# Performance work log

Measured on AMD Instinct MI355X. Metric: run time of the kernel, lower is better.

The kernel has to match this reference:

```python
import jax, jax.numpy as jnp
import numpy as np
from jax import lax

B, T, F0 = 16, 400, 40
H = 512
E = 512
MSQ = H * H  # 262144


def relu20(v):
    return jnp.clip(v, 0.0, 20.0)


def bn3d(x, g, b, eps=1e-5):
    # BatchNorm1d over (B, T) per channel, training-mode batch stats (biased var)
    m = x.mean(axis=(0, 2), keepdims=True)
    v = x.var(axis=(0, 2), keepdims=True)
    return g[None, :, None] * (x - m) / jnp.sqrt(v + eps) + b[None, :, None]


def bn2d(x, g, b, eps=1e-5):
    m = x.mean(axis=0)
    v = x.var(axis=0)
    return g * (x - m) / jnp.sqrt(v + eps) + b


def conv1d(x, w, b, dil):
    # x: [B,C,T], w: [O,I,K] (torch Conv1d layout), VALID padding
    y = lax.conv_general_dilated(x, w, window_strides=(1,), padding='VALID',
                                 rhs_dilation=(dil,),
                                 dimension_numbers=('NCH', 'OIH', 'NCH'))
    return y + b[None, :, None]


def pointwise(x, w, b):
    # nn.Linear applied per timestep; w: [out,in]
    return jnp.einsum('bct,dc->bdt', x, w) + b[None, :, None]


def setup_inputs():
    key = jax.random.key(0)
    ks = jax.random.split(key, 16)
    s = 0.05
    rn = lambda k, shape: jax.random.normal(k, shape, jnp.float32) * s
    inp = {
        'input_x': jax.random.normal(ks[0], (B, 1, T, F0), jnp.float32),
        'conv1_w': rn(ks[1], (H, F0, 5)), 'conv1_b': rn(ks[2], (H,)),
        'bn1_g': jnp.ones((H,), jnp.float32), 'bn1_b': jnp.zeros((H,), jnp.float32),
        'conv2_w': rn(ks[3], (H, H, 3)), 'conv2_b': rn(ks[4], (H,)),
        'bn2_g': jnp.ones((H,), jnp.float32), 'bn2_b': jnp.zeros((H,), jnp.float32),
        'conv3_w': rn(ks[5], (H, H, 3)), 'conv3_b': rn(ks[6], (H,)),
        'bn3_g': jnp.ones((H,), jnp.float32), 'bn3_b': jnp.zeros((H,), jnp.float32),
        'lin4_w': rn(ks[7], (H, H)), 'lin4_b': rn(ks[8], (H,)),
        'bn4_g': jnp.ones((H,), jnp.float32), 'bn4_b': jnp.zeros((H,), jnp.float32),
        'lin5_w': rn(ks[9], (H, H)), 'lin5_b': rn(ks[10], (H,)),
        'bn5_g': jnp.ones((H,), jnp.float32), 'bn5_b': jnp.zeros((H,), jnp.float32),
        'bot_w': jax.random.normal(ks[11], (H, MSQ), jnp.float32) * 0.002,
        'bot_b': rn(ks[12], (H,)),
        'bnb_g': jnp.ones((H,), jnp.float32), 'bnb_b': jnp.zeros((H,), jnp.float32),
        'emb_w': rn(ks[13], (E, H)), 'emb_b': rn(ks[14], (E,)),
    }
    return inp


def reference(input_x, conv1_w, conv1_b, bn1_g, bn1_b,
              conv2_w, conv2_b, bn2_g, bn2_b,
              conv3_w, conv3_b, bn3_g, bn3_b,
              lin4_w, lin4_b, bn4_g, bn4_b,
              lin5_w, lin5_b, bn5_g, bn5_b,
              bot_w, bot_b, bnb_g, bnb_b,
              emb_w, emb_b):
    # (B,1,T,F) -> (B,F,T)
    x = jnp.transpose(input_x[:, 0], (0, 2, 1))
    x = relu20(bn3d(conv1d(x, conv1_w, conv1_b, 1), bn1_g, bn1_b))   # [B,H,T-4]
    x = relu20(bn3d(conv1d(x, conv2_w, conv2_b, 2), bn2_g, bn2_b))   # [B,H,T-8]
    x = relu20(bn3d(conv1d(x, conv3_w, conv3_b, 4), bn3_g, bn3_b))   # [B,H,T-16]
    x = relu20(bn3d(pointwise(x, lin4_w, lin4_b), bn4_g, bn4_b))     # [B,H,T']
    xb = relu20(bn3d(pointwise(x, lin5_w, lin5_b), bn5_g, bn5_b))    # [B,H,T']
    # M[b] = sum_t outer(x[b,:,t], xb[b,:,t])  == batched GEMM
    m = jnp.einsum('bit,bjt->bij', x, xb).reshape(x.shape[0], -1)    # [B, H*H]
    h = relu20(bn2d(m @ bot_w.T + bot_b, bnb_g, bnb_b))              # [B,H]
    emb = h @ emb_w.T + emb_b                                        # [B,E]
    norm = jnp.sqrt(jnp.sum(emb * emb, axis=1) + 1e-10)
    return (emb / norm[:, None]) * 10.0
```

## Files before the change

### kernel.cpp

```cpp
#include <hip/hip_runtime.h>
#include <math.h>

#define BB 16
#define T0 400
#define HH 512
#define T1 396
#define T2 392
#define T3 384
#define KBOT 262144

typedef __attribute__((ext_vector_type(8))) short bf16x8;
typedef __attribute__((ext_vector_type(4))) float f32x4;

__device__ __forceinline__ short f2bf(float f) {
  unsigned u = __builtin_bit_cast(unsigned, f);
  u += 0x7fff + ((u >> 16) & 1);
  return (short)(u >> 16);
}

#define OFF_Y1  0u
#define OFF_Y2  3244032u
#define OFF_Y3  6455296u
#define OFF_Y4  9601024u
#define OFF_Y5  12746752u
#define OFF_M   15892480u
#define OFF_P   20086784u
#define OFF_PP  22183936u
#define OFF_H   22249472u
#define OFF_SC  22257664u
#define OFF_WPK 22262784u
#define OFF_XB0 23393280u
#define OFF_XB1 23598080u
#define OFF_XB2 25220096u
#define OFF_XB3 26825728u
#define OFF_XB4 28398592u
#define OFF_X4F 29971456u
#define OFF_X5F 31544320u

#define WP1 0
#define WP2 163840
#define WP3 950272
#define WP4 1736704
#define WP5 1998848

__global__ __launch_bounds__(256) void pack_weights(
    const float* __restrict__ w1, const float* __restrict__ w2,
    const float* __restrict__ w3, const float* __restrict__ w4,
    const float* __restrict__ w5, short* __restrict__ dst) {
  const int nelem[5] = {163840, 786432, 786432, 262144, 262144};
  const int kbv[5]   = {10, 48, 48, 16, 16};
  const int offv[5]  = {WP1, WP2, WP3, WP4, WP5};
  int widx = blockIdx.y;
  int f = blockIdx.x * 256 + threadIdx.x;
  if (f >= nelem[widx]) return;
  int j = f & 7, lane = (f >> 3) & 63, rest = f >> 9;
  int KB = kbv[widx];
  int kb = rest % KB, mt = rest / KB;
  int m = mt * 16 + (lane & 15);
  int k = kb * 32 + (lane >> 4) * 8 + j;
  float v;
  if (widx == 0) {
    int kt = k >> 6, fi = k & 63;
    v = (fi < 40) ? w1[m * 200 + fi * 5 + kt] : 0.f;
  } else if (widx <= 2) {
    const float* w = (widx == 1) ? w2 : w3;
    int kt = k >> 9, c = k & 511;
    v = w[m * 1536 + c * 3 + kt];
  } else {
    const float* w = (widx == 3) ? w4 : w5;
    v = w[m * 512 + k];
  }
  dst[offv[widx] + f] = f2bf(v);
}

__global__ __launch_bounds__(256) void convert_in(
    const float* __restrict__ in, short* __restrict__ xb0) {
  int row = blockIdx.x * 4 + (threadIdx.x >> 6);
  int c = threadIdx.x & 63;
  float v = (c < 40) ? in[row * 40 + c] : 0.f;
  xb0[row * 64 + c] = f2bf(v);
}

template <int KTAPS, int DIL, int TIN, int TOUT, int CIN>
__global__ __launch_bounds__(256) void gemm_mfma(
    const short* __restrict__ Wpk, const short* __restrict__ Xb, float* __restrict__ Y) {
  constexpr int KBTOT = KTAPS * CIN / 32;
  __shared__ short Bfrag[4096];
  int tid = threadIdx.x;
  int sn = tid >> 2;
  int cb0 = (tid & 3) * 16;
  int cb1 = cb0 + 8;
  int n_glob = blockIdx.x * 64 + sn;
  int b = n_glob / TOUT, t = n_glob - b * TOUT;
  const short* xrow = Xb + (b * TIN + t) * CIN;
  int wave = tid >> 6, lane = tid & 63;
  int wm = wave >> 1, wn = wave & 1;
  int mt0 = blockIdx.y * 4 + wm * 2;
  const short* a_base0 = Wpk + mt0 * KBTOT * 512 + lane * 8;
  const short* a_base1 = a_base0 + KBTOT * 512;
  int wo0 = (((cb0 >> 5) * 4 + (sn >> 4)) * 64 + (sn & 15) + 16 * ((cb0 & 31) >> 3)) * 8;
  int wo1 = (((cb1 >> 5) * 4 + (sn >> 4)) * 64 + (sn & 15) + 16 * ((cb1 & 31) >> 3)) * 8;
  int ro = wn * 1024 + lane * 8;
  f32x4 acc00 = {0,0,0,0}, acc01 = {0,0,0,0}, acc10 = {0,0,0,0}, acc11 = {0,0,0,0};
  for (int kt = 0; kt < KTAPS; ++kt) {
    const short* xk = xrow + DIL * kt * CIN;
    for (int c0 = 0; c0 < CIN; c0 += 64) {
      bf16x8 v0 = *(const bf16x8*)(xk + c0 + cb0);
      bf16x8 v1 = *(const bf16x8*)(xk + c0 + cb1);
      *(bf16x8*)&Bfrag[wo0] = v0;
      *(bf16x8*)&Bfrag[wo1] = v1;
      __syncthreads();
      int kbase = (kt * CIN + c0) >> 5;
      #pragma unroll
      for (int ks = 0; ks < 2; ++ks) {
        bf16x8 a0 = *(const bf16x8*)(a_base0 + (kbase + ks) * 512);
        bf16x8 a1 = *(const bf16x8*)(a_base1 + (kbase + ks) * 512);
        bf16x8 b0 = *(const bf16x8*)&Bfrag[ro + ks * 2048];
        bf16x8 b1 = *(const bf16x8*)&Bfrag[ro + ks * 2048 + 512];
        acc00 = __builtin_amdgcn_mfma_f32_16x16x32_bf16(a0, b0, acc00, 0, 0, 0);
        acc01 = __builtin_amdgcn_mfma_f32_16x16x32_bf16(a0, b1, acc01, 0, 0, 0);
        acc10 = __builtin_amdgcn_mfma_f32_16x16x32_bf16(a1, b0, acc10, 0, 0, 0);
        acc11 = __builtin_amdgcn_mfma_f32_16x16x32_bf16(a1, b1, acc11, 0, 0, 0);
      }
      __syncthreads();
    }
  }
  int quad = lane >> 4, nl = lane & 15;
  int mb = blockIdx.y * 64 + wm * 32 + quad * 4;
  int nb = blockIdx.x * 64 + wn * 32;
  *(f32x4*)(Y + (nb + nl) * 512 + mb)           = acc00;
  *(f32x4*)(Y + (nb + 16 + nl) * 512 + mb)      = acc01;
  *(f32x4*)(Y + (nb + nl) * 512 + mb + 16)      = acc10;
  *(f32x4*)(Y + (nb + 16 + nl) * 512 + mb + 16) = acc11;
}

__global__ __launch_bounds__(256) void bn_partial(
    const float* __restrict__ Y, int nrows, float* __restrict__ Pp) {
  int tid = threadIdx.x;
  float s0 = 0, s20 = 0, s1 = 0, s21 = 0;
  for (int r = blockIdx.x; r < nrows; r += 64) {
    float v0 = Y[r * 512 + tid];
    float v1 = Y[r * 512 + tid + 256];
    s0 += v0; s20 = fmaf(v0, v0, s20);
    s1 += v1; s21 = fmaf(v1, v1, s21);
  }
  float* base = Pp + blockIdx.x * 1024;
  base[tid] = s0; base[tid + 256] = s1;
  base[512 + tid] = s20; base[512 + tid + 256] = s21;
}

__global__ __launch_bounds__(512) void bn_final(
    const float* __restrict__ Pp, const float* __restrict__ g,
    const float* __restrict__ beta, float n, float* __restrict__ sc, float* __restrict__ sh) {
  int c = threadIdx.x;
  float S = 0, S2 = 0;
  for (int blk = 0; blk < 64; ++blk) {
    S += Pp[blk * 1024 + c];
    S2 += Pp[blk * 1024 + 512 + c];
  }
  float mean = S / n, var = S2 / n - mean * mean;
  float scale = g[c] * rsqrtf(var + 1e-5f);
  sc[c] = scale;
  sh[c] = beta[c] - mean * scale;
}

__global__ __launch_bounds__(256) void bn_apply_bf(
    const float* __restrict__ Y, const float* __restrict__ sc,
    const float* __restrict__ sh, short* __restrict__ Xb) {
  int idx = (blockIdx.x * 256 + threadIdx.x) * 8;
  int c = idx & 511;
  float4 a = *(const float4*)(Y + idx);
  float4 d = *(const float4*)(Y + idx + 4);
  float4 s0 = *(const float4*)(sc + c);
  float4 s1 = *(const float4*)(sc + c + 4);
  float4 h0 = *(const float4*)(sh + c);
  float4 h1 = *(const float4*)(sh + c + 4);
  bf16x8 o;
  o[0] = f2bf(fminf(fmaxf(fmaf(a.x, s0.x, h0.x), 0.f), 20.f));
  o[1] = f2bf(fminf(fmaxf(fmaf(a.y, s0.y, h0.y), 0.f), 20.f));
  o[2] = f2bf(fminf(fmaxf(fmaf(a.z, s0.z, h0.z), 0.f), 20.f));
  o[3] = f2bf(fminf(fmaxf(fmaf(a.w, s0.w, h0.w), 0.f), 20.f));
  o[4] = f2bf(fminf(fmaxf(fmaf(d.x, s1.x, h1.x), 0.f), 20.f));
  o[5] = f2bf(fminf(fmaxf(fmaf(d.y, s1.y, h1.y), 0.f), 20.f));
  o[6] = f2bf(fminf(fmaxf(fmaf(d.z, s1.z, h1.z), 0.f), 20.f));
  o[7] = f2bf(fminf(fmaxf(fmaf(d.w, s1.w, h1.w), 0.f), 20.f));
  *(bf16x8*)(Xb + idx) = o;
}

__global__ __launch_bounds__(256) void apply_frag(
    const float* __restrict__ Y, const float* __restrict__ sc,
    const float* __restrict__ sh, short* __restrict__ Xf) {
  __shared__ float ysm[64][65];
  int tk = blockIdx.x, it = blockIdx.y, b = blockIdx.z;
  int tid = threadIdx.x;
  int ii = (tid & 15) * 4;
  #pragma unroll
  for (int p = 0; p < 4; ++p) {
    int tt = p * 16 + (tid >> 4);
    *(float4*)&ysm[tt][ii] =
        *(const float4*)(Y + ((b * 384) + tk * 64 + tt) * 512 + it * 64 + ii);
  }
  __syncthreads();
  int i_loc = tid & 63;
  int i = it * 64 + i_loc;
  float scale = sc[i], shift = sh[i];
  int mt = it * 4 + (i_loc >> 4);
  #pragma unroll
  for (int p = 0; p < 2; ++p) {
    int tq = p * 4 + (tid >> 6);
    bf16x8 pk;
    #pragma unroll
    for (int j = 0; j < 8; ++j) {
      float v = fmaf(ysm[tq * 8 + j][i_loc], scale, shift);
      pk[j] = f2bf(fminf(fmaxf(v, 0.f), 20.f));
    }
    int kb = tk * 2 + (tq >> 2);
    int lanew = (i_loc & 15) + 16 * (tq & 3);
    *(bf16x8*)(Xf + (((b * 32 + mt) * 12 + kb) * 64 + lanew) * 8) = pk;
  }
}

__global__ __launch_bounds__(256) void outer_mfma(
    const short* __restrict__ Af, const short* __restrict__ Bf, float* __restrict__ M) {
  int b = blockIdx.z;
  int tid = threadIdx.x, wave = tid >> 6, lane = tid & 63;
  int wm = wave >> 1, wn = wave & 1;
  int mt0 = blockIdx.y * 4 + wm * 2;
  int nt0 = blockIdx.x * 4 + wn * 2;
  const short* pa0 = Af + (b * 32 + mt0) * 12 * 512 + lane * 8;
  const short* pa1 = pa0 + 12 * 512;
  const short* pb0 = Bf + (b * 32 + nt0) * 12 * 512 + lane * 8;
  const short* pb1 = pb0 + 12 * 512;
  f32x4 acc00 = {0,0,0,0}, acc01 = {0,0,0,0}, acc10 = {0,0,0,0}, acc11 = {0,0,0,0};
  #pragma unroll 4
  for (int kb = 0; kb < 12; ++kb) {
    bf16x8 a0 = *(const bf16x8*)(pa0 + kb * 512);
    bf16x8 a1 = *(const bf16x8*)(pa1 + kb * 512);
    bf16x8 b0 = *(const bf16x8*)(pb0 + kb * 512);
    bf16x8 b1 = *(const bf16x8*)(pb1 + kb * 512);
    acc00 = __builtin_amdgcn_mfma_f32_16x16x32_bf16(a0, b0, acc00, 0, 0, 0);
    acc01 = __builtin_amdgcn_mfma_f32_16x16x32_bf16(a0, b1, acc01, 0, 0, 0);
    acc10 = __builtin_amdgcn_mfma_f32_16x16x32_bf16(a1, b0, acc10, 0, 0, 0);
    acc11 = __builtin_amdgcn_mfma_f32_16x16x32_bf16(a1, b1, acc11, 0, 0, 0);
  }
  int quad = lane >> 4, nl = lane & 15;
  float* Mb = M + b * 262144;
  int i0 = blockIdx.y * 64 + wm * 32 + quad * 4;
  int j0 = blockIdx.x * 64 + wn * 32 + nl;
  #pragma unroll
  for (int r = 0; r < 4; ++r) {
    Mb[(i0 + r) * 512 + j0]           = acc00[r];
    Mb[(i0 + r) * 512 + j0 + 16]      = acc01[r];
    Mb[(i0 + 16 + r) * 512 + j0]      = acc10[r];
    Mb[(i0 + 16 + r) * 512 + j0 + 16] = acc11[r];
  }
}

__global__ __launch_bounds__(256) void bot_partial_kernel(
    const float* __restrict__ m, const float* __restrict__ W, float* __restrict__ P) {
  __shared__ float Ws[32][128];
  __shared__ float Ms[32][16];
  int ic = blockIdx.x;
  int n0 = blockIdx.y * 128;
  int tid = threadIdx.x;
  int kb = ic * 1024;
  int wr = tid >> 1;
  int wc = (tid & 1) * 16;
  int nl = (tid & 63) * 2;
  int bq = (tid >> 6) * 4;
  float acc[4][2] = {};
  for (int k0 = kb; k0 < kb + 1024; k0 += 32) {
    #pragma unroll
    for (int q = 0; q < 4; ++q) {
      float4 wv = *(const float4*)(W + (n0 + wr) * KBOT + k0 + wc + q * 4);
      Ws[wc + q * 4 + 0][wr] = wv.x; Ws[wc + q * 4 + 1][wr] = wv.y;
      Ws[wc + q * 4 + 2][wr] = wv.z; Ws[wc + q * 4 + 3][wr] = wv.w;
    }
    if (tid < 128) {
      int b = tid >> 3, kg = (tid & 7) * 4;
      float4 mv = *(const float4*)(m + b * KBOT + k0 + kg);
      Ms[kg + 0][b] = mv.x; Ms[kg + 1][b] = mv.y; Ms[kg + 2][b] = mv.z; Ms[kg + 3][b] = mv.w;
    }
    __syncthreads();
    #pragma unroll
    for (int kk = 0; kk < 32; ++kk) {
      float2 w2 = *(const float2*)&Ws[kk][nl];
      float4 m4 = *(const float4*)&Ms[kk][bq];
      acc[0][0] = fmaf(m4.x, w2.x, acc[0][0]); acc[0][1] = fmaf(m4.x, w2.y, acc[0][1]);
      acc[1][0] = fmaf(m4.y, w2.x, acc[1][0]); acc[1][1] = fmaf(m4.y, w2.y, acc[1][1]);
      acc[2][0] = fmaf(m4.z, w2.x, acc[2][0]); acc[2][1] = fmaf(m4.z, w2.y, acc[2][1]);
      acc[3][0] = fmaf(m4.w, w2.x, acc[3][0]); acc[3][1] = fmaf(m4.w, w2.y, acc[3][1]);
    }
    __syncthreads();
  }
  #pragma unroll
  for (int i = 0; i < 4; ++i) {
    float* row = P + (ic * 16 + bq + i) * 512 + n0;
    *(float2*)&row[nl] = make_float2(acc[i][0], acc[i][1]);
  }
}

__global__ __launch_bounds__(256) void bot_reduce_kernel(
    const float* __restrict__ P, float* __restrict__ h) {
  int idx = blockIdx.x * 256 + threadIdx.x;
  float s[8] = {};
  for (int ic = 0; ic < 256; ic += 8) {
    #pragma unroll
    for (int q = 0; q < 8; ++q) s[q] += P[(ic + q) * 8192 + idx];
  }
  h[idx] = ((s[0] + s[1]) + (s[2] + s[3])) + ((s[4] + s[5]) + (s[6] + s[7]));
}

__global__ __launch_bounds__(512) void final_kernel(
    const float* __restrict__ h, const float* __restrict__ gb, const float* __restrict__ bb,
    const float* __restrict__ embw, const float* __restrict__ embb, float* __restrict__ out) {
  __shared__ float hn[512];
  __shared__ float red[8];
  int b = blockIdx.x, e = threadIdx.x;
  float s = 0.f, s2 = 0.f;
  #pragma unroll
  for (int q = 0; q < BB; ++q) {
    float v = h[q * 512 + e];
    s += v; s2 = fmaf(v, v, s2);
  }
  float mean = s * (1.f / BB);
  float var = s2 * (1.f / BB) - mean * mean;
  float scale = gb[e] * rsqrtf(var + 1e-5f);
  float val = fmaf(h[b * 512 + e] - mean, scale, bb[e]);
  hn[e] = fminf(fmaxf(val, 0.f), 20.f);
  __syncthreads();
  float acc = 0.f;
  const float* wr = embw + e * 512;
  for (int c = 0; c < 512; c += 4) {
    float4 w4 = *(const float4*)(wr + c);
    float4 h4 = *(const float4*)&hn[c];
    acc = fmaf(w4.x, h4.x, acc); acc = fmaf(w4.y, h4.y, acc);
    acc = fmaf(w4.z, h4.z, acc); acc = fmaf(w4.w, h4.w, acc);
  }
  acc += embb[e];
  float sq = acc * acc;
  #pragma unroll
  for (int off = 32; off > 0; off >>= 1) sq += __shfl_down(sq, off);
  if ((e & 63) == 0) red[e >> 6] = sq;
  __syncthreads();
  float tot = 0.f;
  #pragma unroll
  for (int q = 0; q < 8; ++q) tot += red[q];
  float norm = sqrtf(tot + 1e-10f);
  out[b * 512 + e] = acc * (10.f / norm);
}

extern "C" void kernel_launch(void* const* d_in, const int* in_sizes, int n_in,
                              void* d_out, int out_size, void* d_ws, size_t ws_size,
                              hipStream_t stream) {
  const float* input_x = (const float*)d_in[0];
  const float* w1 = (const float*)d_in[1];
  const float* g1 = (const float*)d_in[3];  const float* b1 = (const float*)d_in[4];
  const float* w2 = (const float*)d_in[5];
  const float* g2 = (const float*)d_in[7];  const float* b2 = (const float*)d_in[8];
  const float* w3 = (const float*)d_in[9];
  const float* g3 = (const float*)d_in[11]; const float* b3 = (const float*)d_in[12];
  const float* w4 = (const float*)d_in[13];
  const float* g4 = (const float*)d_in[15]; const float* b4 = (const float*)d_in[16];
  const float* w5 = (const float*)d_in[17];
  const float* g5 = (const float*)d_in[19]; const float* b5 = (const float*)d_in[20];
  const float* botw = (const float*)d_in[21];
  const float* gb = (const float*)d_in[23]; const float* bb = (const float*)d_in[24];
  const float* embw = (const float*)d_in[25]; const float* embb = (const float*)d_in[26];

  float* ws = (float*)d_ws;
  float* y1 = ws + OFF_Y1;
  float* y2 = ws + OFF_Y2;
  float* y3 = ws + OFF_Y3;
  float* y4 = ws + OFF_Y4;
  float* y5 = ws + OFF_Y5;
  float* M  = ws + OFF_M;
  float* P  = ws + OFF_P;
  float* Pp = ws + OFF_PP;
  float* h  = ws + OFF_H;
  float* SC = ws + OFF_SC;
  short* WPK = (short*)(ws + OFF_WPK);
  short* xb0 = (short*)(ws + OFF_XB0);
  short* xb1 = (short*)(ws + OFF_XB1);
  short* xb2 = (short*)(ws + OFF_XB2);
  short* xb3 = (short*)(ws + OFF_XB3);
  short* xb4 = (short*)(ws + OFF_XB4);
  short* x4f = (short*)(ws + OFF_X4F);
  short* x5f = (short*)(ws + OFF_X5F);
  float* out = (float*)d_out;

  pack_weights<<<dim3(3072, 5), 256, 0, stream>>>(w1, w2, w3, w4, w5, WPK);
  convert_in<<<1600, 256, 0, stream>>>(input_x, xb0);

  gemm_mfma<5, 1, 400, 396, 64><<<dim3(99, 8), 256, 0, stream>>>(WPK + WP1, xb0, y1);
  bn_partial<<<64, 256, 0, stream>>>(y1, 6336, Pp);
  bn_final<<<1, 512, 0, stream>>>(Pp, g1, b1, 6336.f, SC + 0, SC + 512);
  bn_apply_bf<<<1584, 256, 0, stream>>>(y1, SC + 0, SC + 512, xb1);

  gemm_mfma<3, 2, 396, 392, 512><<<dim3(98, 8), 256, 0, stream>>>(WPK + WP2, xb1, y2);
  bn_partial<<<64, 256, 0, stream>>>(y2, 6272, Pp);
  bn_final<<<1, 512, 0, stream>>>(Pp, g2, b2, 6272.f, SC + 1024, SC + 1536);
  bn_apply_bf<<<1568, 256, 0, stream>>>(y2, SC + 1024, SC + 1536, xb2);

  gemm_mfma<3, 4, 392, 384, 512><<<dim3(96, 8), 256, 0, stream>>>(WPK + WP3, xb2, y3);
  bn_partial<<<64, 256, 0, stream>>>(y3, 6144, Pp);
  bn_final<<<1, 512, 0, stream>>>(Pp, g3, b3, 6144.f, SC + 2048, SC + 2560);
  bn_apply_bf<<<1536, 256, 0, stream>>>(y3, SC + 2048, SC + 2560, xb3);

  gemm_mfma<1, 0, 384, 384, 512><<<dim3(96, 8), 256, 0, stream>>>(WPK + WP4, xb3, y4);
  bn_partial<<<64, 256, 0, stream>>>(y4, 6144, Pp);
  bn_final<<<1, 512, 0, stream>>>(Pp, g4, b4, 6144.f, SC + 3072, SC + 3584);
  bn_apply_bf<<<1536, 256, 0, stream>>>(y4, SC + 3072, SC + 3584, xb4);

  gemm_mfma<1, 0, 384, 384, 512><<<dim3(96, 8), 256, 0, stream>>>(WPK + WP5, xb4, y5);
  bn_partial<<<64, 256, 0, stream>>>(y5, 6144, Pp);
  bn_final<<<1, 512, 0, stream>>>(Pp, g5, b5, 6144.f, SC + 4096, SC + 4608);

  apply_frag<<<dim3(6, 8, 16), 256, 0, stream>>>(y4, SC + 3072, SC + 3584, x4f);
  apply_frag<<<dim3(6, 8, 16), 256, 0, stream>>>(y5, SC + 4096, SC + 4608, x5f);

  outer_mfma<<<dim3(8, 8, 16), 256, 0, stream>>>(x4f, x5f, M);
  bot_partial_kernel<<<dim3(256, 4), 256, 0, stream>>>(M, botw, P);
  bot_reduce_kernel<<<32, 256, 0, stream>>>(P, h);
  final_kernel<<<16, 512, 0, stream>>>(h, gb, bb, embw, embb, out);
}
```

Measured before the change: 1.093 ms.

## Fuse BN statistics into GEMM epilogue, double-buffer GEMM, prefetch bottleneck loads

The conv/pointwise GEMMs now reduce per-channel sum and sum-of-squares in their epilogue and write per-block partials. A last-block-done atomic counter lets the final block compute BN scale and shift, which removes the separate bn_partial and bn_final launches and their re-read of Y. The GEMM main loop is double-buffered in LDS with register prefetch of the next A/B fragments, and the two apply_frag launches are merged into one grid. The bottleneck partial kernel also prefetches the next W/M tile into registers before the inner FMA loop. The trade-offs are an extra threadfence and atomic per GEMM block, and a serial tail where one block reduces all partials.

```diff
diff --git a/kernel.cpp b/kernel.cpp
--- a/kernel.cpp
+++ b/kernel.cpp
@@ -74,7 +74,8 @@
 }
 
 __global__ __launch_bounds__(256) void convert_in(
-    const float* __restrict__ in, short* __restrict__ xb0) {
+    const float* __restrict__ in, short* __restrict__ xb0, unsigned* __restrict__ cnt) {
+  if (blockIdx.x == 0 && threadIdx.x == 0) *cnt = 0u;
   int row = blockIdx.x * 4 + (threadIdx.x >> 6);
   int c = threadIdx.x & 63;
   float v = (c < 40) ? in[row * 40 + c] : 0.f;
@@ -83,9 +84,14 @@
 
 template <int KTAPS, int DIL, int TIN, int TOUT, int CIN>
 __global__ __launch_bounds__(256) void gemm_mfma(
-    const short* __restrict__ Wpk, const short* __restrict__ Xb, float* __restrict__ Y) {
+    const short* __restrict__ Wpk, const short* __restrict__ Xb, float* __restrict__ Y,
+    float* __restrict__ Ps, unsigned* __restrict__ cnt,
+    const float* __restrict__ g, const float* __restrict__ beta, float nfull,
+    float* __restrict__ sc, float* __restrict__ sh) {
   constexpr int KBTOT = KTAPS * CIN / 32;
-  __shared__ short Bfrag[4096];
+  constexpr int NIT = KTAPS * CIN / 64;
+  constexpr int CSEG = CIN / 64;
+  __shared__ short Bfrag[2][4096];
   int tid = threadIdx.x;
   int sn = tid >> 2;
   int cb0 = (tid & 3) * 16;
@@ -102,66 +108,125 @@
   int wo1 = (((cb1 >> 5) * 4 + (sn >> 4)) * 64 + (sn & 15) + 16 * ((cb1 & 31) >> 3)) * 8;
   int ro = wn * 1024 + lane * 8;
   f32x4 acc00 = {0,0,0,0}, acc01 = {0,0,0,0}, acc10 = {0,0,0,0}, acc11 = {0,0,0,0};
-  for (int kt = 0; kt < KTAPS; ++kt) {
-    const short* xk = xrow + DIL * kt * CIN;
-    for (int c0 = 0; c0 < CIN; c0 += 64) {
-      bf16x8 v0 = *(const bf16x8*)(xk + c0 + cb0);
-      bf16x8 v1 = *(const bf16x8*)(xk + c0 + cb1);
-      *(bf16x8*)&Bfrag[wo0] = v0;
-      *(bf16x8*)&Bfrag[wo1] = v1;
-      __syncthreads();
-      int kbase = (kt * CIN + c0) >> 5;
-      #pragma unroll
-      for (int ks = 0; ks < 2; ++ks) {
-        bf16x8 a0 = *(const bf16x8*)(a_base0 + (kbase + ks) * 512);
-        bf16x8 a1 = *(const bf16x8*)(a_base1 + (kbase + ks) * 512);
-        bf16x8 b0 = *(const bf16x8*)&Bfrag[ro + ks * 2048];
-        bf16x8 b1 = *(const bf16x8*)&Bfrag[ro + ks * 2048 + 512];
-        acc00 = __builtin_amdgcn_mfma_f32_16x16x32_bf16(a0, b0, acc00, 0, 0, 0);
-        acc01 = __builtin_amdgcn_mfma_f32_16x16x32_bf16(a0, b1, acc01, 0, 0, 0);
-        acc10 = __builtin_amdgcn_mfma_f32_16x16x32_bf16(a1, b0, acc10, 0, 0, 0);
-        acc11 = __builtin_amdgcn_mfma_f32_16x16x32_bf16(a1, b1, acc11, 0, 0, 0);
-      }
-      __syncthreads();
-    }
-  }
+
+  bf16x8 a00 = *(const bf16x8*)(a_base0);
+  bf16x8 a01 = *(const bf16x8*)(a_base0 + 512);
+  bf16x8 a10 = *(const bf16x8*)(a_base1);
+  bf16x8 a11 = *(const bf16x8*)(a_base1 + 512);
+  {
+    bf16x8 v0 = *(const bf16x8*)(xrow + cb0);
+    bf16x8 v1 = *(const bf16x8*)(xrow + cb1);
+    *(bf16x8*)&Bfrag[0][wo0] = v0;
+    *(bf16x8*)&Bfrag[0][wo1] = v1;
+  }
+  __syncthreads();
+  int cur = 0;
+  #pragma unroll
+  for (int it = 0; it < NIT; ++it) {
+    bf16x8 nv0, nv1, na00, na01, na10, na11;
+    const bool more = (it + 1 < NIT);
+    if (more) {
+      int it1 = it + 1;
+      int kt = it1 / CSEG;
+      int c0 = (it1 - kt * CSEG) * 64;
+      const short* p = xrow + DIL * kt * CIN + c0;
+      nv0 = *(const bf16x8*)(p + cb0);
+      nv1 = *(const bf16x8*)(p + cb1);
+      const short* ab0 = a_base0 + it1 * 1024;
+      const short* ab1 = a_base1 + it1 * 1024;
+      na00 = *(const bf16x8*)(ab0);
+      na01 = *(const bf16x8*)(ab0 + 512);
+      na10 = *(const bf16x8*)(ab1);
+      na11 = *(const bf16x8*)(ab1 + 512);
+    }
+    short* bf = &Bfrag[cur][0];
+    bf16x8 bk0n0 = *(const bf16x8*)(bf + ro);
+    bf16x8 bk0n1 = *(const bf16x8*)(bf + ro + 512);
+    bf16x8 bk1n0 = *(const bf16x8*)(bf + ro + 2048);
+    bf16x8 bk1n1 = *(const bf16x8*)(bf + ro + 2560);
+    acc00 = __builtin_amdgcn_mfma_f32_16x16x32_bf16(a00, bk0n0, acc00, 0, 0, 0);
+    acc01 = __builtin_amdgcn_mfma_f32_16x16x32_bf16(a00, bk0n1, acc01, 0, 0, 0);
+    acc10 = __builtin_amdgcn_mfma_f32_16x16x32_bf16(a10, bk0n0, acc10, 0, 0, 0);
+    acc11 = __builtin_amdgcn_mfma_f32_16x16x32_bf16(a10, bk0n1, acc11, 0, 0, 0);
+    acc00 = __builtin_amdgcn_mfma_f32_16x16x32_bf16(a01, bk1n0, acc00, 0, 0, 0);
+    acc01 = __builtin_amdgcn_mfma_f32_16x16x32_bf16(a01, bk1n1, acc01, 0, 0, 0);
+    acc10 = __builtin_amdgcn_mfma_f32_16x16x32_bf16(a11, bk1n0, acc10, 0, 0, 0);
+    acc11 = __builtin_amdgcn_mfma_f32_16x16x32_bf16(a11, bk1n1, acc11, 0, 0, 0);
+    if (more) {
+      *(bf16x8*)&Bfrag[cur ^ 1][wo0] = nv0;
+      *(bf16x8*)&Bfrag[cur ^ 1][wo1] = nv1;
+      a00 = na00; a01 = na01; a10 = na10; a11 = na11;
+    }
+    __syncthreads();
+    cur ^= 1;
+  }
+
   int quad = lane >> 4, nl = lane & 15;
-  int mb = blockIdx.y * 64 + wm * 32 + quad * 4;
-  int nb = blockIdx.x * 64 + wn * 32;
-  *(f32x4*)(Y + (nb + nl) * 512 + mb)           = acc00;
-  *(f32x4*)(Y + (nb + 16 + nl) * 512 + mb)      = acc01;
-  *(f32x4*)(Y + (nb + nl) * 512 + mb + 16)      = acc10;
-  *(f32x4*)(Y + (nb + 16 + nl) * 512 + mb + 16) = acc11;
-}
-
-__global__ __launch_bounds__(256) void bn_partial(
-    const float* __restrict__ Y, int nrows, float* __restrict__ Pp) {
-  int tid = threadIdx.x;
-  float s0 = 0, s20 = 0, s1 = 0, s21 = 0;
-  for (int r = blockIdx.x; r < nrows; r += 64) {
-    float v0 = Y[r * 512 + tid];
-    float v1 = Y[r * 512 + tid + 256];
-    s0 += v0; s20 = fmaf(v0, v0, s20);
-    s1 += v1; s21 = fmaf(v1, v1, s21);
-  }
-  float* base = Pp + blockIdx.x * 1024;
-  base[tid] = s0; base[tid + 256] = s1;
-  base[512 + tid] = s20; base[512 + tid + 256] = s21;
-}
-
-__global__ __launch_bounds__(512) void bn_final(
-    const float* __restrict__ Pp, const float* __restrict__ g,
-    const float* __restrict__ beta, float n, float* __restrict__ sc, float* __restrict__ sh) {
-  int c = threadIdx.x;
-  float S = 0, S2 = 0;
-  for (int blk = 0; blk < 64; ++blk) {
-    S += Pp[blk * 1024 + c];
-    S2 += Pp[blk * 1024 + 512 + c];
-  }
-  float mean = S / n, var = S2 / n - mean * mean;
-  float scale = g[c] * rsqrtf(var + 1e-5f);
-  sc[c] = scale;
-  sh[c] = beta[c] - mean * scale;
+  int chq = wm * 32 + quad * 4;
+  int mbase = blockIdx.y * 64 + chq;
+  int nb0 = blockIdx.x * 64 + wn * 32;
+  *(f32x4*)(Y + (nb0 + nl) * 512 + mbase)           = acc00;
+  *(f32x4*)(Y + (nb0 + 16 + nl) * 512 + mbase)      = acc01;
+  *(f32x4*)(Y + (nb0 + nl) * 512 + mbase + 16)      = acc10;
+  *(f32x4*)(Y + (nb0 + 16 + nl) * 512 + mbase + 16) = acc11;
+
+  float cs0[4], cq0[4], cs1[4], cq1[4];
+  #pragma unroll
+  for (int r = 0; r < 4; ++r) {
+    cs0[r] = acc00[r] + acc01[r];
+    cq0[r] = acc00[r] * acc00[r] + acc01[r] * acc01[r];
+    cs1[r] = acc10[r] + acc11[r];
+    cq1[r] = acc10[r] * acc10[r] + acc11[r] * acc11[r];
+  }
+  #pragma unroll
+  for (int off = 1; off < 16; off <<= 1) {
+    #pragma unroll
+    for (int r = 0; r < 4; ++r) {
+      cs0[r] += __shfl_xor(cs0[r], off);
+      cq0[r] += __shfl_xor(cq0[r], off);
+      cs1[r] += __shfl_xor(cs1[r], off);
+      cq1[r] += __shfl_xor(cq1[r], off);
+    }
+  }
+  if (nl == 0) {
+    float* prow = Ps + (blockIdx.x * 2 + wn) * 1024 + mbase;
+    #pragma unroll
+    for (int r = 0; r < 4; ++r) {
+      prow[r] = cs0[r];
+      prow[16 + r] = cs1[r];
+      prow[512 + r] = cq0[r];
+      prow[528 + r] = cq1[r];
+    }
+  }
+  __threadfence();
+  __syncthreads();
+  __shared__ unsigned s_done;
+  if (tid == 0)
+    s_done = __hip_atomic_fetch_add(cnt, 1u, __ATOMIC_ACQ_REL, __HIP_MEMORY_SCOPE_AGENT);
+  __syncthreads();
+  unsigned nblk = gridDim.x * gridDim.y;
+  if (s_done == nblk - 1) {
+    __threadfence();
+    if (tid == 0) *cnt = 0u;
+    int npr = gridDim.x * 2;
+    int c = tid * 2;
+    float Sx = 0.f, Sy = 0.f, Qx = 0.f, Qy = 0.f;
+    for (int r2 = 0; r2 < npr; ++r2) {
+      const float* pr = Ps + r2 * 1024;
+      float2 a = *(const float2*)(pr + c);
+      float2 q = *(const float2*)(pr + 512 + c);
+      Sx += a.x; Sy += a.y; Qx += q.x; Qy += q.y;
+    }
+    float inv_n = 1.f / nfull;
+    float mx = Sx * inv_n, my = Sy * inv_n;
+    float vx = Qx * inv_n - mx * mx;
+    float vy = Qy * inv_n - my * my;
+    float scx = g[c] * rsqrtf(vx + 1e-5f);
+    float scy = g[c + 1] * rsqrtf(vy + 1e-5f);
+    sc[c] = scx; sc[c + 1] = scy;
+    sh[c] = beta[c] - mx * scx;
+    sh[c + 1] = beta[c + 1] - my * scy;
+  }
 }
 
 __global__ __launch_bounds__(256) void bn_apply_bf(
@@ -188,10 +253,16 @@
 }
 
 __global__ __launch_bounds__(256) void apply_frag(
-    const float* __restrict__ Y, const float* __restrict__ sc,
-    const float* __restrict__ sh, short* __restrict__ Xf) {
+    const float* __restrict__ Y4, const float* __restrict__ Y5,
+    const float* __restrict__ SCb, short* __restrict__ X4f, short* __restrict__ X5f) {
   __shared__ float ysm[64][65];
-  int tk = blockIdx.x, it = blockIdx.y, b = blockIdx.z;
+  int tk = blockIdx.x, it = blockIdx.y;
+  int sel = blockIdx.z >> 4;
+  int b = blockIdx.z & 15;
+  const float* Y = sel ? Y5 : Y4;
+  const float* scp = SCb + (sel ? 4096 : 3072);
+  const float* shp = scp + 512;
+  short* Xf = sel ? X5f : X4f;
   int tid = threadIdx.x;
   int ii = (tid & 15) * 4;
   #pragma unroll
@@ -203,7 +274,7 @@
   __syncthreads();
   int i_loc = tid & 63;
   int i = it * 64 + i_loc;
-  float scale = sc[i], shift = sh[i];
+  float scale = scp[i], shift = shp[i];
   int mt = it * 4 + (i_loc >> 4);
   #pragma unroll
   for (int p = 0; p < 2; ++p) {
@@ -268,20 +339,35 @@
   int wc = (tid & 1) * 16;
   int nl = (tid & 63) * 2;
   int bq = (tid >> 6) * 4;
+  int mrow = tid >> 3, mkg = (tid & 7) * 4;
+  const float* wrow = W + (n0 + wr) * KBOT;
+  const float* mrowp = m + mrow * KBOT;
   float acc[4][2] = {};
+  float4 wbuf[4];
+  float4 mbuf = make_float4(0.f, 0.f, 0.f, 0.f);
+  #pragma unroll
+  for (int q = 0; q < 4; ++q) wbuf[q] = *(const float4*)(wrow + kb + wc + q * 4);
+  if (tid < 128) mbuf = *(const float4*)(mrowp + kb + mkg);
   for (int k0 = kb; k0 < kb + 1024; k0 += 32) {
     #pragma unroll
     for (int q = 0; q < 4; ++q) {
-      float4 wv = *(const float4*)(W + (n0 + wr) * KBOT + k0 + wc + q * 4);
-      Ws[wc + q * 4 + 0][wr] = wv.x; Ws[wc + q * 4 + 1][wr] = wv.y;
-      Ws[wc + q * 4 + 2][wr] = wv.z; Ws[wc + q * 4 + 3][wr] = wv.w;
+      Ws[wc + q * 4 + 0][wr] = wbuf[q].x;
+      Ws[wc + q * 4 + 1][wr] = wbuf[q].y;
+      Ws[wc + q * 4 + 2][wr] = wbuf[q].z;
+      Ws[wc + q * 4 + 3][wr] = wbuf[q].w;
     }
     if (tid < 128) {
-      int b = tid >> 3, kg = (tid & 7) * 4;
-      float4 mv = *(const float4*)(m + b * KBOT + k0 + kg);
-      Ms[kg + 0][b] = mv.x; Ms[kg + 1][b] = mv.y; Ms[kg + 2][b] = mv.z; Ms[kg + 3][b] = mv.w;
+      Ms[mkg + 0][mrow] = mbuf.x;
+      Ms[mkg + 1][mrow] = mbuf.y;
+      Ms[mkg + 2][mrow] = mbuf.z;
+      Ms[mkg + 3][mrow] = mbuf.w;
     }
     __syncthreads();
+    if (k0 + 32 < kb + 1024) {
+      #pragma unroll
+      for (int q = 0; q < 4; ++q) wbuf[q] = *(const float4*)(wrow + k0 + 32 + wc + q * 4);
+      if (tid < 128) mbuf = *(const float4*)(mrowp + k0 + 32 + mkg);
+    }
     #pragma unroll
     for (int kk = 0; kk < 32; ++kk) {
       float2 w2 = *(const float2*)&Ws[kk][nl];
@@ -376,7 +462,8 @@
   float* y5 = ws + OFF_Y5;
   float* M  = ws + OFF_M;
   float* P  = ws + OFF_P;
-  float* Pp = ws + OFF_PP;
+  float* Ps = ws + OFF_P;
+  unsigned* cnt = (unsigned*)(ws + OFF_PP);
   float* h  = ws + OFF_H;
   float* SC = ws + OFF_SC;
   short* WPK = (short*)(ws + OFF_WPK);
@@ -390,34 +477,28 @@
   float* out = (float*)d_out;
 
   pack_weights<<<dim3(3072, 5), 256, 0, stream>>>(w1, w2, w3, w4, w5, WPK);
-  convert_in<<<1600, 256, 0, stream>>>(input_x, xb0);
-
-  gemm_mfma<5, 1, 400, 396, 64><<<dim3(99, 8), 256, 0, stream>>>(WPK + WP1, xb0, y1);
-  bn_partial<<<64, 256, 0, stream>>>(y1, 6336, Pp);
-  bn_final<<<1, 512, 0, stream>>>(Pp, g1, b1, 6336.f, SC + 0, SC + 512);
+  convert_in<<<1600, 256, 0, stream>>>(input_x, xb0, cnt);
+
+  gemm_mfma<5, 1, 400, 396, 64><<<dim3(99, 8), 256, 0, stream>>>(
+      WPK + WP1, xb0, y1, Ps, cnt, g1, b1, 6336.f, SC + 0, SC + 512);
   bn_apply_bf<<<1584, 256, 0, stream>>>(y1, SC + 0, SC + 512, xb1);
 
-  gemm_mfma<3, 2, 396, 392, 512><<<dim3(98, 8), 256, 0, stream>>>(WPK + WP2, xb1, y2);
-  bn_partial<<<64, 256, 0, stream>>>(y2, 6272, Pp);
-  bn_final<<<1, 512, 0, stream>>>(Pp, g2, b2, 6272.f, SC + 1024, SC + 1536);
+  gemm_mfma<3, 2, 396, 392, 512><<<dim3(98, 8), 256, 0, stream>>>(
+      WPK + WP2, xb1, y2, Ps, cnt, g2, b2, 6272.f, SC + 1024, SC + 1536);
   bn_apply_bf<<<1568, 256, 0, stream>>>(y2, SC + 1024, SC + 1536, xb2);
 
-  gemm_mfma<3, 4, 392, 384, 512><<<dim3(96, 8), 256, 0, stream>>>(WPK + WP3, xb2, y3);
-  bn_partial<<<64, 256, 0, stream>>>(y3, 6144, Pp);
-  bn_final<<<1, 512, 0, stream>>>(Pp, g3, b3, 6144.f, SC + 2048, SC + 2560);
+  gemm_mfma<3, 4, 392, 384, 512><<<dim3(96, 8), 256, 0, stream>>>(
+      WPK + WP3, xb2, y3, Ps, cnt, g3, b3, 6144.f, SC + 2048, SC + 2560);
   bn_apply_bf<<<1536, 256, 0, stream>>>(y3, SC + 2048, SC + 2560, xb3);
 
-  gemm_mfma<1, 0, 384, 384, 512><<<dim3(96, 8), 256, 0, stream>>>(WPK + WP4, xb3, y4);
-  bn_partial<<<64, 256, 0, stream>>>(y4, 6144, Pp);
-  bn_final<<<1, 512, 0, stream>>>(Pp, g4, b4, 6144.f, SC + 3072, SC + 3584);
+  gemm_mfma<1, 0, 384, 384, 512><<<dim3(96, 8), 256, 0, stream>>>(
+      WPK + WP4, xb3, y4, Ps, cnt, g4, b4, 6144.f, SC + 3072, SC + 3584);
   bn_apply_bf<<<1536, 256, 0, stream>>>(y4, SC + 3072, SC + 3584, xb4);
 
-  gemm_mfma<1, 0, 384, 384, 512><<<dim3(96, 8), 256, 0, stream>>>(WPK + WP5, xb4, y5);
-  bn_partial<<<64, 256, 0, stream>>>(y5, 6144, Pp);
-  bn_final<<<1, 512, 0, stream>>>(Pp, g5, b5, 6144.f, SC + 4096, SC + 4608);
-
-  apply_frag<<<dim3(6, 8, 16), 256, 0, stream>>>(y4, SC + 3072, SC + 3584, x4f);
-  apply_frag<<<dim3(6, 8, 16), 256, 0, stream>>>(y5, SC + 4096, SC + 4608, x5f);
+  gemm_mfma<1, 0, 384, 384, 512><<<dim3(96, 8), 256, 0, stream>>>(
+      WPK + WP5, xb4, y5, Ps, cnt, g5, b5, 6144.f, SC + 4096, SC + 4608);
+
+  apply_frag<<<dim3(6, 8, 32), 256, 0, stream>>>(y4, y5, SC, x4f, x5f);
 
   outer_mfma<<<dim3(8, 8, 16), 256, 0, stream>>>(x4f, x5f, M);
   bot_partial_kernel<<<dim3(256, 4), 256, 0, stream>>>(M, botw, P);
```

Result: slower. 1.623 ms (+48.6%).
